# Kernel tuning notes

Measured on AMD Instinct MI355X. Metric: run time of the kernel, lower is better.

Reference implementation:

```python
import jax, jax.numpy as jnp
import numpy as np

B, N, C = 4, 2048, 3
IN_DIM, OUT_DIM, H = 128, 128, 4
D = OUT_DIM // H  # d_head = 32
NEG_INF = -1e9


def setup_inputs() -> dict:
    key = jax.random.key(0)
    k_h, k_adj, k_W, k_a, k_Wo, k_bo = jax.random.split(key, 6)
    h = jax.random.normal(k_h, (B, N, IN_DIM), dtype=jnp.float32)
    adj = jax.random.normal(k_adj, (B, C, N, N), dtype=jnp.float32)
    # params (xavier-ish scales)
    W = jax.random.normal(k_W, (IN_DIM, OUT_DIM), dtype=jnp.float32) * (1.0 / np.sqrt(IN_DIM))
    a = jax.random.normal(k_a, (H, 2 * D), dtype=jnp.float32) * (1.0 / np.sqrt(2 * D))
    a_src, a_dst = a[:, :D], a[:, D:]
    Wo = jax.random.normal(k_Wo, (OUT_DIM, OUT_DIM), dtype=jnp.float32) * (1.0 / np.sqrt(OUT_DIM))
    bo = jnp.zeros((OUT_DIM,), dtype=jnp.float32)
    return {"h": h, "adj": adj, "W": W, "a_src": a_src, "a_dst": a_dst, "Wo": Wo, "bo": bo}


def reference(h, adj, W, a_src, a_dst, Wo, bo):
    b, n, _ = h.shape
    # Wh: [B, N, H, D]
    Wh = jnp.einsum('bni,io->bno', h, W).reshape(b, n, H, D)
    # additive attention score decomposed: e[b,h,i,j] = lrelu(a_src.Wh_i + a_dst.Wh_j)
    src = jnp.einsum('bnhd,hd->bhn', Wh, a_src)  # [B,H,N]
    dst = jnp.einsum('bnhd,hd->bhn', Wh, a_dst)  # [B,H,N]
    e = jax.nn.leaky_relu(src[:, :, :, None] + dst[:, :, None, :], negative_slope=0.2)  # [B,H,N,N]
    # mask from multi-channel adjacency: [B,1,N,N]
    mask = (jnp.mean(adj, axis=1, keepdims=True) > 0).astype(e.dtype)
    e = e * mask + (1.0 - mask) * NEG_INF
    alpha = jax.nn.softmax(e, axis=-1)  # dropout is identity in eval mode
    # weighted sum over j: out[b,i,h,d] = sum_j alpha[b,h,i,j] * Wh[b,j,h,d]
    out = jnp.einsum('bhij,bjhd->bihd', alpha, Wh).reshape(b, n, OUT_DIM)
    return jax.nn.elu(out @ Wo + bo)
```

## Files before the change

kernel.cpp:

```cpp
#include <hip/hip_runtime.h>
#include <hip/hip_bf16.h>
#include <math.h>

#define BB 4
#define NN 2048
#define CC 3
#define HH 4
#define DD 32

typedef __attribute__((ext_vector_type(8))) short bf16x8;
typedef __attribute__((ext_vector_type(4))) float f32x4;

__device__ inline unsigned short f2bf(float x) {
    __hip_bfloat16 b = __float2bfloat16(x);
    return __builtin_bit_cast(unsigned short, b);
}

__global__ __launch_bounds__(256) void k1_wh(const float* __restrict__ h,
                                             const float* __restrict__ W,
                                             const float* __restrict__ a_src,
                                             const float* __restrict__ a_dst,
                                             float* __restrict__ Wh,
                                             float* __restrict__ srcv,
                                             float* __restrict__ dstv) {
    __shared__ float hrow[2][128];
    int tid = threadIdx.x;
    int r = tid >> 7, c = tid & 127;
    int row = blockIdx.x * 2 + r;
    int b = row >> 11;
    int n = row & 2047;
    hrow[r][c] = h[row * 128 + c];
    __syncthreads();
    float acc = 0.f;
#pragma unroll
    for (int k = 0; k < 128; ++k)
        acc = fmaf(hrow[r][k], W[k * 128 + c], acc);
    Wh[row * 128 + c] = acc;
    float ps = acc * a_src[c];
    float pd = acc * a_dst[c];
#pragma unroll
    for (int m = 16; m >= 1; m >>= 1) {
        ps += __shfl_xor(ps, m);
        pd += __shfl_xor(pd, m);
    }
    if ((c & 31) == 0) {
        int hh = c >> 5;
        srcv[(b * HH + hh) * NN + n] = ps;
        dstv[(b * HH + hh) * NN + n] = pd;
    }
}

__global__ __launch_bounds__(256) void k1t(const float* __restrict__ Wh,
                                           unsigned short* __restrict__ WhT) {
    int tid = threadIdx.x;
    int wave = tid >> 6, lane = tid & 63;
    int blk = blockIdx.x;
    int jb = blk & 15;
    int dgrp = (blk >> 4) & 1;
    int bh = blk >> 5;
    int b = bh >> 2, hh = bh & 3;
    int d = dgrp * 16 + (lane & 15);
    int jc = jb * 128 + wave * 32 + (lane >> 4) * 8;
    const float* src = Wh + ((long long)(b * NN + jc)) * 128 + hh * 32 + d;
    bf16x8 v;
#pragma unroll
    for (int i = 0; i < 8; ++i)
        v[i] = (short)f2bf(src[i * 128]);
    *(bf16x8*)&WhT[((long long)bh * 32 + d) * NN + jc] = v;
}

__global__ __launch_bounds__(256) void k2_mask(const float* __restrict__ adj,
                                               const float* __restrict__ dstv,
                                               unsigned* __restrict__ maskb32,
                                               float* __restrict__ dmax) {
    __shared__ float dl[HH][NN];
    int tid = threadIdx.x;
    int rowg0 = blockIdx.x * 4;
    int b = rowg0 >> 11;
    {
        const float4* s4 = (const float4*)(dstv + (long long)b * HH * NN);
        float4* d4 = (float4*)&dl[0][0];
        for (int idx = tid; idx < HH * NN / 4; idx += 256) d4[idx] = s4[idx];
    }
    __syncthreads();
    int wave = tid >> 6, lane = tid & 63;
    int i = (rowg0 & 2047) + wave;
    const float* a0 = adj + ((long long)(b * CC + 0) * NN + i) * NN;
    const float* a1 = adj + ((long long)(b * CC + 1) * NN + i) * NN;
    const float* a2 = adj + ((long long)(b * CC + 2) * NN + i) * NN;
    float m0 = -INFINITY, m1 = -INFINITY, m2 = -INFINITY, m3 = -INFINITY;
    for (int jt = 0; jt < 8; ++jt) {
        int j4 = jt * 256 + lane * 4;
        float4 f0 = *(const float4*)&a0[j4];
        float4 f1 = *(const float4*)&a1[j4];
        float4 f2 = *(const float4*)&a2[j4];
        unsigned nib = (unsigned)(f0.x + f1.x + f2.x > 0.f) |
                       ((unsigned)(f0.y + f1.y + f2.y > 0.f) << 1) |
                       ((unsigned)(f0.z + f1.z + f2.z > 0.f) << 2) |
                       ((unsigned)(f0.w + f1.w + f2.w > 0.f) << 3);
        unsigned w = nib << (4 * (lane & 7));
        w |= __shfl_xor((int)w, 1);
        w |= __shfl_xor((int)w, 2);
        w |= __shfl_xor((int)w, 4);
        if ((lane & 7) == 0) maskb32[((long long)b * NN + i) * 64 + (j4 >> 5)] = w;
#pragma unroll
        for (int hh = 0; hh < HH; ++hh) {
            float4 dv4 = ((const float4*)&dl[hh][0])[jt * 64 + lane];
            float a = (nib & 1) ? dv4.x : -INFINITY;
            float bb2 = (nib & 2) ? dv4.y : -INFINITY;
            float cc2 = (nib & 4) ? dv4.z : -INFINITY;
            float dd2 = (nib & 8) ? dv4.w : -INFINITY;
            float mx = fmaxf(fmaxf(a, bb2), fmaxf(cc2, dd2));
            if (hh == 0) m0 = fmaxf(m0, mx);
            if (hh == 1) m1 = fmaxf(m1, mx);
            if (hh == 2) m2 = fmaxf(m2, mx);
            if (hh == 3) m3 = fmaxf(m3, mx);
        }
    }
#pragma unroll
    for (int m = 32; m >= 1; m >>= 1) {
        m0 = fmaxf(m0, __shfl_xor(m0, m));
        m1 = fmaxf(m1, __shfl_xor(m1, m));
        m2 = fmaxf(m2, __shfl_xor(m2, m));
        m3 = fmaxf(m3, __shfl_xor(m3, m));
    }
    if (lane == 0) {
        dmax[(b * HH + 0) * NN + i] = m0;
        dmax[(b * HH + 1) * NN + i] = m1;
        dmax[(b * HH + 2) * NN + i] = m2;
        dmax[(b * HH + 3) * NN + i] = m3;
    }
}

__global__ __launch_bounds__(256) void k3_attn(const unsigned short* __restrict__ WhT,
                                               const float* __restrict__ srcv,
                                               const float* __restrict__ dstv,
                                               const float* __restrict__ dmax,
                                               const unsigned* __restrict__ maskb32,
                                               float* __restrict__ part,
                                               float* __restrict__ plsum) {
    int tid = threadIdx.x;
    int wave = tid >> 6, lane = tid & 63;
    int blk = blockIdx.x;
    int jh = blk & 1;
    int rest = blk >> 1;
    int it = rest & 31;
    int bh = rest >> 5;
    int b = bh >> 2;
    int r = lane & 15, kg = lane >> 4;
    long long bhN = (long long)bh * NN;
    int row = it * 64 + wave * 16 + r;

    float s = srcv[bhN + row];
    float dm = dmax[bhN + row];
    bool allm = !(dm > -INFINITY);
    float e0 = s + dm;
    float m = e0 > 0.f ? e0 : 0.2f * e0;
    if (allm) m = 0.f;

    const unsigned* mrow = maskb32 + ((long long)b * NN + row) * 64;
    const unsigned short* wb = WhT + (long long)bh * 32 * NN;
    const unsigned short* w0 = wb + (long long)r * NN;
    const unsigned short* w1 = wb + (long long)(16 + r) * NN;

    f32x4 acc0 = {0.f, 0.f, 0.f, 0.f};
    f32x4 acc1 = {0.f, 0.f, 0.f, 0.f};
    float psum = 0.f;

    for (int t = 0; t < 32; ++t) {
        unsigned mw = mrow[jh * 32 + t];
        int jk = jh * 1024 + t * 32 + kg * 8;
        float4 dva = *(const float4*)&dstv[bhN + jk];
        float4 dvb = *(const float4*)&dstv[bhN + jk + 4];
        float dvs[8] = {dva.x, dva.y, dva.z, dva.w, dvb.x, dvb.y, dvb.z, dvb.w};
        bf16x8 af;
#pragma unroll
        for (int i = 0; i < 8; ++i) {
            float e = s + dvs[i];
            float lr = e > 0.f ? e : 0.2f * e;
            bool bit = (mw >> (kg * 8 + i)) & 1u;
            float p = allm ? 1.f : (bit ? __expf(lr - m) : 0.f);
            psum += p;
            af[i] = (short)f2bf(p);
        }
        bf16x8 bf0 = *(const bf16x8*)&w0[jk];
        bf16x8 bf1 = *(const bf16x8*)&w1[jk];
        acc0 = __builtin_amdgcn_mfma_f32_16x16x32_bf16(af, bf0, acc0, 0, 0, 0);
        acc1 = __builtin_amdgcn_mfma_f32_16x16x32_bf16(af, bf1, acc1, 0, 0, 0);
    }

    psum += __shfl_xor(psum, 16);
    psum += __shfl_xor(psum, 32);

    long long pbase = (long long)blk * 64 + wave * 16;
#pragma unroll
    for (int reg = 0; reg < 4; ++reg) {
        int rl = kg * 4 + reg;
        part[(pbase + rl) * 32 + r] = acc0[reg];
        part[(pbase + rl) * 32 + 16 + r] = acc1[reg];
    }
    if (kg == 0) plsum[pbase + r] = psum;
}

__global__ __launch_bounds__(256) void k3_reduce(const float* __restrict__ part,
                                                 const float* __restrict__ plsum,
                                                 float* __restrict__ attn) {
    int g = blockIdx.x * 256 + threadIdx.x;
    int d4 = g & 7;
    int r = (g >> 3) & 63;
    int it = (g >> 9) & 31;
    int bh = g >> 14;
    int b = bh >> 2, hh = bh & 3;
    int tile0 = (bh * 32 + it) * 2;
    const float4 p0 = *(const float4*)&part[((long long)tile0 * 64 + r) * 32 + d4 * 4];
    const float4 p1 = *(const float4*)&part[((long long)(tile0 + 1) * 64 + r) * 32 + d4 * 4];
    float l = plsum[tile0 * 64 + r] + plsum[(tile0 + 1) * 64 + r];
    float inv = 1.f / l;
    float4 o;
    o.x = (p0.x + p1.x) * inv;
    o.y = (p0.y + p1.y) * inv;
    o.z = (p0.z + p1.z) * inv;
    o.w = (p0.w + p1.w) * inv;
    int n = it * 64 + r;
    *(float4*)&attn[((long long)(b * NN + n) * 128) + hh * 32 + d4 * 4] = o;
}

__global__ __launch_bounds__(256) void k4_out(const float* __restrict__ attn,
                                              const float* __restrict__ Wo,
                                              const float* __restrict__ bo,
                                              float* __restrict__ out) {
    __shared__ float arow[2][128];
    int tid = threadIdx.x;
    int r = tid >> 7, c = tid & 127;
    int row = blockIdx.x * 2 + r;
    arow[r][c] = attn[row * 128 + c];
    __syncthreads();
    float acc = bo[c];
#pragma unroll
    for (int k = 0; k < 128; ++k)
        acc = fmaf(arow[r][k], Wo[k * 128 + c], acc);
    out[row * 128 + c] = acc > 0.f ? acc : expm1f(acc);
}

extern "C" void kernel_launch(void* const* d_in, const int* in_sizes, int n_in,
                              void* d_out, int out_size, void* d_ws, size_t ws_size,
                              hipStream_t stream) {
    const float* h     = (const float*)d_in[0];
    const float* adj   = (const float*)d_in[1];
    const float* W     = (const float*)d_in[2];
    const float* a_src = (const float*)d_in[3];
    const float* a_dst = (const float*)d_in[4];
    const float* Wo    = (const float*)d_in[5];
    const float* bo    = (const float*)d_in[6];
    float* out = (float*)d_out;

    char* ws = (char*)d_ws;
    float* Wh    = (float*)(ws);
    float* attn  = (float*)(ws + (4 << 20));
    float* srcv  = (float*)(ws + (8 << 20));
    float* dstv  = (float*)(ws + (8 << 20) + (128 << 10));
    float* dmax  = (float*)(ws + (8 << 20) + (256 << 10));
    unsigned* maskb32 = (unsigned*)(ws + (8 << 20) + (384 << 10));
    float* part  = (float*)(ws + (10 << 20) + (384 << 10));
    float* plsum = (float*)(ws + (18 << 20) + (384 << 10));
    unsigned short* WhT = (unsigned short*)(ws + (18 << 20) + (640 << 10));

    k1_wh<<<dim3(BB * NN / 2), dim3(256), 0, stream>>>(h, W, a_src, a_dst, Wh, srcv, dstv);
    k1t<<<dim3(512), dim3(256), 0, stream>>>(Wh, WhT);
    k2_mask<<<dim3(BB * NN / 4), dim3(256), 0, stream>>>(adj, dstv, maskb32, dmax);
    k3_attn<<<dim3(BB * HH * (NN / 64) * 2), dim3(256), 0, stream>>>(WhT, srcv, dstv, dmax,
                                                                     maskb32, part, plsum);
    k3_reduce<<<dim3(1024), dim3(256), 0, stream>>>(part, plsum, attn);
    k4_out<<<dim3(BB * NN / 2), dim3(256), 0, stream>>>(attn, Wo, bo, out);
}
```

Before: 390.2 us.

## Fuse split-K reduce into output GEMM, register-tile projections, drop LDS staging in mask

The partial-sum reduction and normalization move into the output projection kernel, which removes one launch and the attn intermediate round trip. Both small 128x128 GEMM kernels now process 8 rows per block, with each thread computing a 2x2 output tile using float2 weight loads, which cuts redundant weight reads. The mask kernel no longer copies the full per-batch dst vector into shared memory for every block and reads it directly from global/cache instead. The gather in k4 uses scattered scalar loads from the part buffer, so it may coalesce poorly.

Result: slower. 405.2 us (+3.8%).

```diff
diff --git a/kernel.cpp b/kernel.cpp
--- a/kernel.cpp
+++ b/kernel.cpp
@@ -23,30 +23,53 @@
                                              float* __restrict__ Wh,
                                              float* __restrict__ srcv,
                                              float* __restrict__ dstv) {
-    __shared__ float hrow[2][128];
-    int tid = threadIdx.x;
-    int r = tid >> 7, c = tid & 127;
-    int row = blockIdx.x * 2 + r;
-    int b = row >> 11;
-    int n = row & 2047;
-    hrow[r][c] = h[row * 128 + c];
+    __shared__ float hrow[8][128];
+    int tid = threadIdx.x;
+    int row0 = blockIdx.x * 8;
+    int b = row0 >> 11;
+    {
+        int rr = tid >> 5, k4 = (tid & 31) * 4;
+        *(float4*)&hrow[rr][k4] = *(const float4*)&h[(long long)(row0 + rr) * 128 + k4];
+    }
     __syncthreads();
-    float acc = 0.f;
-#pragma unroll
-    for (int k = 0; k < 128; ++k)
-        acc = fmaf(hrow[r][k], W[k * 128 + c], acc);
-    Wh[row * 128 + c] = acc;
-    float ps = acc * a_src[c];
-    float pd = acc * a_dst[c];
-#pragma unroll
-    for (int m = 16; m >= 1; m >>= 1) {
-        ps += __shfl_xor(ps, m);
-        pd += __shfl_xor(pd, m);
-    }
-    if ((c & 31) == 0) {
-        int hh = c >> 5;
-        srcv[(b * HH + hh) * NN + n] = ps;
-        dstv[(b * HH + hh) * NN + n] = pd;
+    int c2 = tid & 63;
+    int r2 = tid >> 6;
+    int c0 = c2 * 2;
+    const float* h0p = hrow[r2 * 2];
+    const float* h1p = hrow[r2 * 2 + 1];
+    float a00 = 0.f, a01 = 0.f, a10 = 0.f, a11 = 0.f;
+#pragma unroll
+    for (int k = 0; k < 128; ++k) {
+        float2 w = *(const float2*)&W[k * 128 + c0];
+        float h0 = h0p[k], h1 = h1p[k];
+        a00 = fmaf(h0, w.x, a00);
+        a01 = fmaf(h0, w.y, a01);
+        a10 = fmaf(h1, w.x, a10);
+        a11 = fmaf(h1, w.y, a11);
+    }
+    long long rowA = row0 + r2 * 2, rowB = rowA + 1;
+    *(float2*)&Wh[rowA * 128 + c0] = make_float2(a00, a01);
+    *(float2*)&Wh[rowB * 128 + c0] = make_float2(a10, a11);
+    float as0 = a_src[c0], as1 = a_src[c0 + 1];
+    float ad0 = a_dst[c0], ad1 = a_dst[c0 + 1];
+    float ps0 = a00 * as0 + a01 * as1;
+    float pd0 = a00 * ad0 + a01 * ad1;
+    float ps1 = a10 * as0 + a11 * as1;
+    float pd1 = a10 * ad0 + a11 * ad1;
+#pragma unroll
+    for (int m = 1; m <= 8; m <<= 1) {
+        ps0 += __shfl_xor(ps0, m);
+        pd0 += __shfl_xor(pd0, m);
+        ps1 += __shfl_xor(ps1, m);
+        pd1 += __shfl_xor(pd1, m);
+    }
+    if ((c2 & 15) == 0) {
+        int hh = c2 >> 4;
+        int nA = (row0 & 2047) + r2 * 2;
+        srcv[(b * HH + hh) * NN + nA] = ps0;
+        dstv[(b * HH + hh) * NN + nA] = pd0;
+        srcv[(b * HH + hh) * NN + nA + 1] = ps1;
+        dstv[(b * HH + hh) * NN + nA + 1] = pd1;
     }
 }
 
@@ -73,21 +96,17 @@
                                                const float* __restrict__ dstv,
                                                unsigned* __restrict__ maskb32,
                                                float* __restrict__ dmax) {
-    __shared__ float dl[HH][NN];
-    int tid = threadIdx.x;
-    int rowg0 = blockIdx.x * 4;
-    int b = rowg0 >> 11;
-    {
-        const float4* s4 = (const float4*)(dstv + (long long)b * HH * NN);
-        float4* d4 = (float4*)&dl[0][0];
-        for (int idx = tid; idx < HH * NN / 4; idx += 256) d4[idx] = s4[idx];
-    }
-    __syncthreads();
+    int tid = threadIdx.x;
     int wave = tid >> 6, lane = tid & 63;
-    int i = (rowg0 & 2047) + wave;
-    const float* a0 = adj + ((long long)(b * CC + 0) * NN + i) * NN;
-    const float* a1 = adj + ((long long)(b * CC + 1) * NN + i) * NN;
-    const float* a2 = adj + ((long long)(b * CC + 2) * NN + i) * NN;
+    int i = blockIdx.x * 4 + wave;
+    int b = i >> 11, il = i & 2047;
+    const float* a0 = adj + ((long long)(b * CC + 0) * NN + il) * NN;
+    const float* a1 = adj + ((long long)(b * CC + 1) * NN + il) * NN;
+    const float* a2 = adj + ((long long)(b * CC + 2) * NN + il) * NN;
+    const float4* dh0 = (const float4*)(dstv + (long long)(b * HH + 0) * NN);
+    const float4* dh1 = (const float4*)(dstv + (long long)(b * HH + 1) * NN);
+    const float4* dh2 = (const float4*)(dstv + (long long)(b * HH + 2) * NN);
+    const float4* dh3 = (const float4*)(dstv + (long long)(b * HH + 3) * NN);
     float m0 = -INFINITY, m1 = -INFINITY, m2 = -INFINITY, m3 = -INFINITY;
     for (int jt = 0; jt < 8; ++jt) {
         int j4 = jt * 256 + lane * 4;
@@ -102,20 +121,17 @@
         w |= __shfl_xor((int)w, 1);
         w |= __shfl_xor((int)w, 2);
         w |= __shfl_xor((int)w, 4);
-        if ((lane & 7) == 0) maskb32[((long long)b * NN + i) * 64 + (j4 >> 5)] = w;
-#pragma unroll
-        for (int hh = 0; hh < HH; ++hh) {
-            float4 dv4 = ((const float4*)&dl[hh][0])[jt * 64 + lane];
-            float a = (nib & 1) ? dv4.x : -INFINITY;
-            float bb2 = (nib & 2) ? dv4.y : -INFINITY;
-            float cc2 = (nib & 4) ? dv4.z : -INFINITY;
-            float dd2 = (nib & 8) ? dv4.w : -INFINITY;
-            float mx = fmaxf(fmaxf(a, bb2), fmaxf(cc2, dd2));
-            if (hh == 0) m0 = fmaxf(m0, mx);
-            if (hh == 1) m1 = fmaxf(m1, mx);
-            if (hh == 2) m2 = fmaxf(m2, mx);
-            if (hh == 3) m3 = fmaxf(m3, mx);
-        }
+        if ((lane & 7) == 0) maskb32[((long long)b * NN + il) * 64 + (j4 >> 5)] = w;
+        int q = jt * 64 + lane;
+        float4 v0 = dh0[q], v1 = dh1[q], v2 = dh2[q], v3 = dh3[q];
+        m0 = fmaxf(m0, fmaxf(fmaxf((nib & 1) ? v0.x : -INFINITY, (nib & 2) ? v0.y : -INFINITY),
+                             fmaxf((nib & 4) ? v0.z : -INFINITY, (nib & 8) ? v0.w : -INFINITY)));
+        m1 = fmaxf(m1, fmaxf(fmaxf((nib & 1) ? v1.x : -INFINITY, (nib & 2) ? v1.y : -INFINITY),
+                             fmaxf((nib & 4) ? v1.z : -INFINITY, (nib & 8) ? v1.w : -INFINITY)));
+        m2 = fmaxf(m2, fmaxf(fmaxf((nib & 1) ? v2.x : -INFINITY, (nib & 2) ? v2.y : -INFINITY),
+                             fmaxf((nib & 4) ? v2.z : -INFINITY, (nib & 8) ? v2.w : -INFINITY)));
+        m3 = fmaxf(m3, fmaxf(fmaxf((nib & 1) ? v3.x : -INFINITY, (nib & 2) ? v3.y : -INFINITY),
+                             fmaxf((nib & 4) ? v3.z : -INFINITY, (nib & 8) ? v3.w : -INFINITY)));
     }
 #pragma unroll
     for (int m = 32; m >= 1; m >>= 1) {
@@ -125,10 +141,10 @@
         m3 = fmaxf(m3, __shfl_xor(m3, m));
     }
     if (lane == 0) {
-        dmax[(b * HH + 0) * NN + i] = m0;
-        dmax[(b * HH + 1) * NN + i] = m1;
-        dmax[(b * HH + 2) * NN + i] = m2;
-        dmax[(b * HH + 3) * NN + i] = m3;
+        dmax[(b * HH + 0) * NN + il] = m0;
+        dmax[(b * HH + 1) * NN + il] = m1;
+        dmax[(b * HH + 2) * NN + il] = m2;
+        dmax[(b * HH + 3) * NN + il] = m3;
     }
 }
 
@@ -202,44 +218,54 @@
     if (kg == 0) plsum[pbase + r] = psum;
 }
 
-__global__ __launch_bounds__(256) void k3_reduce(const float* __restrict__ part,
-                                                 const float* __restrict__ plsum,
-                                                 float* __restrict__ attn) {
-    int g = blockIdx.x * 256 + threadIdx.x;
-    int d4 = g & 7;
-    int r = (g >> 3) & 63;
-    int it = (g >> 9) & 31;
-    int bh = g >> 14;
-    int b = bh >> 2, hh = bh & 3;
-    int tile0 = (bh * 32 + it) * 2;
-    const float4 p0 = *(const float4*)&part[((long long)tile0 * 64 + r) * 32 + d4 * 4];
-    const float4 p1 = *(const float4*)&part[((long long)(tile0 + 1) * 64 + r) * 32 + d4 * 4];
-    float l = plsum[tile0 * 64 + r] + plsum[(tile0 + 1) * 64 + r];
-    float inv = 1.f / l;
-    float4 o;
-    o.x = (p0.x + p1.x) * inv;
-    o.y = (p0.y + p1.y) * inv;
-    o.z = (p0.z + p1.z) * inv;
-    o.w = (p0.w + p1.w) * inv;
-    int n = it * 64 + r;
-    *(float4*)&attn[((long long)(b * NN + n) * 128) + hh * 32 + d4 * 4] = o;
-}
-
-__global__ __launch_bounds__(256) void k4_out(const float* __restrict__ attn,
+__global__ __launch_bounds__(256) void k4_out(const float* __restrict__ part,
+                                              const float* __restrict__ plsum,
                                               const float* __restrict__ Wo,
                                               const float* __restrict__ bo,
                                               float* __restrict__ out) {
-    __shared__ float arow[2][128];
-    int tid = threadIdx.x;
-    int r = tid >> 7, c = tid & 127;
-    int row = blockIdx.x * 2 + r;
-    arow[r][c] = attn[row * 128 + c];
+    __shared__ float arow[8][128];
+    int tid = threadIdx.x;
+    int row0 = blockIdx.x * 8;
+    int b = row0 >> 11;
+#pragma unroll
+    for (int q = 0; q < 4; ++q) {
+        int li = q * 256 + tid;
+        int rr = li >> 7, c = li & 127;
+        int row = row0 + rr;
+        int nn = row & 2047;
+        int it = nn >> 6, rl = nn & 63;
+        int hh = c >> 5, d = c & 31;
+        int bh = b * HH + hh;
+        long long t0 = (long long)(bh * 32 + it) * 2;
+        float p0 = part[(t0 * 64 + rl) * 32 + d];
+        float p1 = part[((t0 + 1) * 64 + rl) * 32 + d];
+        float l = plsum[t0 * 64 + rl] + plsum[(t0 + 1) * 64 + rl];
+        arow[rr][c] = (p0 + p1) / l;
+    }
     __syncthreads();
-    float acc = bo[c];
-#pragma unroll
-    for (int k = 0; k < 128; ++k)
-        acc = fmaf(arow[r][k], Wo[k * 128 + c], acc);
-    out[row * 128 + c] = acc > 0.f ? acc : expm1f(acc);
+    int c2 = tid & 63;
+    int r2 = tid >> 6;
+    int c0 = c2 * 2;
+    const float* h0p = arow[r2 * 2];
+    const float* h1p = arow[r2 * 2 + 1];
+    float a00 = bo[c0], a01 = bo[c0 + 1];
+    float a10 = a00, a11 = a01;
+#pragma unroll
+    for (int k = 0; k < 128; ++k) {
+        float2 w = *(const float2*)&Wo[k * 128 + c0];
+        float h0 = h0p[k], h1 = h1p[k];
+        a00 = fmaf(h0, w.x, a00);
+        a01 = fmaf(h0, w.y, a01);
+        a10 = fmaf(h1, w.x, a10);
+        a11 = fmaf(h1, w.y, a11);
+    }
+    long long rowA = row0 + r2 * 2, rowB = rowA + 1;
+    float o00 = a00 > 0.f ? a00 : expm1f(a00);
+    float o01 = a01 > 0.f ? a01 : expm1f(a01);
+    float o10 = a10 > 0.f ? a10 : expm1f(a10);
+    float o11 = a11 > 0.f ? a11 : expm1f(a11);
+    *(float2*)&out[rowA * 128 + c0] = make_float2(o00, o01);
+    *(float2*)&out[rowB * 128 + c0] = make_float2(o10, o11);
 }
 
 extern "C" void kernel_launch(void* const* d_in, const int* in_sizes, int n_in,
@@ -256,7 +282,6 @@
 
     char* ws = (char*)d_ws;
     float* Wh    = (float*)(ws);
-    float* attn  = (float*)(ws + (4 << 20));
     float* srcv  = (float*)(ws + (8 << 20));
     float* dstv  = (float*)(ws + (8 << 20) + (128 << 10));
     float* dmax  = (float*)(ws + (8 << 20) + (256 << 10));
@@ -265,11 +290,10 @@
     float* plsum = (float*)(ws + (18 << 20) + (384 << 10));
     unsigned short* WhT = (unsigned short*)(ws + (18 << 20) + (640 << 10));
 
-    k1_wh<<<dim3(BB * NN / 2), dim3(256), 0, stream>>>(h, W, a_src, a_dst, Wh, srcv, dstv);
+    k1_wh<<<dim3(1024), dim3(256), 0, stream>>>(h, W, a_src, a_dst, Wh, srcv, dstv);
     k1t<<<dim3(512), dim3(256), 0, stream>>>(Wh, WhT);
     k2_mask<<<dim3(BB * NN / 4), dim3(256), 0, stream>>>(adj, dstv, maskb32, dmax);
     k3_attn<<<dim3(BB * HH * (NN / 64) * 2), dim3(256), 0, stream>>>(WhT, srcv, dstv, dmax,
                                                                      maskb32, part, plsum);
-    k3_reduce<<<dim3(1024), dim3(256), 0, stream>>>(part, plsum, attn);
-    k4_out<<<dim3(BB * NN / 2), dim3(256), 0, stream>>>(attn, Wo, bo, out);
-}
+    k4_out<<<dim3(1024), dim3(256), 0, stream>>>(part, plsum, Wo, bo, out);
+}
```
